# Kernel tuning notes

Measured on AMD Instinct MI355X. Metric: run time of the kernel, lower is better.

The kernel has to match this reference:

```python
import jax, jax.numpy as jnp
import numpy as np

B, CIN, F, H, W = 4, 256, 128, 64, 64
EPS = 1e-5

def _conv1x1(x, Wm, b):
    # x: [B,C,H,W], Wm: [O,C] (1x1 conv kernel), b: [O]
    return jnp.einsum('bchw,oc->bohw', x, Wm) + b[None, :, None, None]

def setup_inputs() -> dict:
    key = jax.random.key(0)
    ks = jax.random.split(key, 11)
    s_in = 1.0 / np.sqrt(CIN)
    s_f = 1.0 / np.sqrt(F)
    return {
        'x':    jax.random.normal(ks[0], (B, CIN, H, W), jnp.float32),
        'Wg':   jax.random.normal(ks[1], (F, CIN), jnp.float32) * s_in,
        'bg':   jax.random.normal(ks[2], (F,), jnp.float32) * s_in,
        'Wt':   jax.random.normal(ks[3], (F, CIN), jnp.float32) * s_in,
        'bt':   jax.random.normal(ks[4], (F,), jnp.float32) * s_in,
        'Wp':   jax.random.normal(ks[5], (F, CIN), jnp.float32) * s_in,
        'bp':   jax.random.normal(ks[6], (F,), jnp.float32) * s_in,
        'Wz':   jax.random.normal(ks[7], (CIN, F), jnp.float32) * s_f,
        'bz':   jax.random.normal(ks[8], (CIN,), jnp.float32) * s_f,
        'ln_w': jax.random.normal(ks[9], (CIN, H, W), jnp.float32) * 0.1,
        'ln_b': jax.random.normal(ks[10], (CIN, H, W), jnp.float32) * 0.1,
    }

def reference(x, Wg, bg, Wt, bt, Wp, bp, Wz, bz, ln_w, ln_b):
    b, _, h, w = x.shape
    n = h * w
    # 1x1 conv projections
    g = _conv1x1(x, Wg, bg).reshape(b, F, n).transpose(0, 2, 1)      # [B,N,F]
    theta = _conv1x1(x, Wt, bt).reshape(b, F, n).transpose(0, 2, 1)  # [B,N,F]
    phi = _conv1x1(x, Wp, bp).reshape(b, F, n)                        # [B,F,N]
    # embedded-Gaussian affinity + softmax attention
    f = jnp.einsum('bnf,bfm->bnm', theta, phi)                        # [B,N,N]
    attn = jax.nn.softmax(f, axis=-1)
    y = jnp.einsum('bnm,bmf->bnf', attn, g)                           # [B,N,F]
    y = y.transpose(0, 2, 1).reshape(b, F, h, w)                      # [B,F,H,W]
    # output projection
    z = _conv1x1(y, Wz, bz)                                           # [B,CIN,H,W]
    # LayerNorm over (C,H,W) per sample, affine params shaped [C,H,W]
    mu = jnp.mean(z, axis=(1, 2, 3), keepdims=True)
    var = jnp.var(z, axis=(1, 2, 3), keepdims=True)
    z = (z - mu) * jax.lax.rsqrt(var + EPS)
    z = z * ln_w[None] + ln_b[None]
    return z + x
```

## Files before the change

### kernel.cpp

```cpp
#include <hip/hip_runtime.h>
#include <stdint.h>

#define CIN 256
#define FDIM 128
#define NSP 4096
#define EPS 1e-5f

typedef __attribute__((ext_vector_type(8))) short short8;
typedef __attribute__((ext_vector_type(4))) float f32x4;
typedef __attribute__((ext_vector_type(16))) float f32x16;

__device__ __forceinline__ short f2bf(float f) {
  union { float f; uint32_t u; } v; v.f = f;
  uint32_t r = v.u + 0x7fffu + ((v.u >> 16) & 1u);
  return (short)(r >> 16);
}
__device__ __forceinline__ float bf2f(short h) {
  union { uint32_t u; float f; } v; v.u = ((uint32_t)(uint16_t)h) << 16;
  return v.f;
}

__global__ void prep_weights(const float* __restrict__ Wg, const float* __restrict__ Wt,
                             const float* __restrict__ Wp, const float* __restrict__ Wz,
                             short* __restrict__ Wbf, short* __restrict__ Wzbf) {
  int idx = blockIdx.x * 256 + threadIdx.x;
  if (idx < 384 * 256) {
    int row = idx >> 8, col = idx & 255;
    float v;
    if (row < 128)       v = Wt[row * 256 + col];
    else if (row < 256)  v = Wp[(row - 128) * 256 + col];
    else                 v = Wg[(row - 256) * 256 + col];
    Wbf[idx] = f2bf(v);
  } else {
    int j = idx - 384 * 256;
    if (j < 256 * 128) Wzbf[j] = f2bf(Wz[j]);
  }
}

__global__ void prep_xT(const float* __restrict__ x, short* __restrict__ xT) {
  __shared__ float tile[32][33];
  int b = blockIdx.z, c0 = blockIdx.y * 32, n0 = blockIdx.x * 32;
  int r = threadIdx.x >> 5, c = threadIdx.x & 31;
  const float* xb = x + (size_t)b * CIN * NSP;
#pragma unroll
  for (int k = 0; k < 4; k++)
    tile[r + 8 * k][c] = xb[(size_t)(c0 + r + 8 * k) * NSP + n0 + c];
  __syncthreads();
  short* xTb = xT + (size_t)b * NSP * CIN;
#pragma unroll
  for (int k = 0; k < 4; k++)
    xTb[(size_t)(n0 + r + 8 * k) * CIN + c0 + c] = f2bf(tile[c][r + 8 * k]);
}

__global__ void __launch_bounds__(256)
proj_kernel(const short* __restrict__ xT, const short* __restrict__ Wbf,
            const float* __restrict__ bt, const float* __restrict__ bp,
            const float* __restrict__ bg,
            short* __restrict__ theta, short* __restrict__ Kb, short* __restrict__ gT) {
  __shared__ short lds[5120];
  int bx = blockIdx.x;
  int b = bx >> 7;
  int n0 = (bx & 127) << 5;
  int p = blockIdx.y;
  int t = threadIdx.x, w = t >> 6, lane = t & 63, l15 = lane & 15, quad = lane >> 4;

  const short* arow = xT + (size_t)(b * NSP + n0 + (w & 1) * 16 + l15) * CIN;
  short8 a[8];
#pragma unroll
  for (int s = 0; s < 8; s++) a[s] = *(const short8*)(arow + s * 32 + quad * 8);

  const short* Wsrc = Wbf + p * 128 * 256;
  f32x4 zero = {0.f, 0.f, 0.f, 0.f};
  f32x4 acc[4];
#pragma unroll
  for (int i = 0; i < 4; i++) acc[i] = zero;

#pragma unroll
  for (int s = 0; s < 8; s++) {
#pragma unroll
    for (int ft = 0; ft < 4; ft++) {
      int ftg = (w >> 1) * 4 + ft;
      short8 bfr = *(const short8*)(Wsrc + (ftg * 16 + l15) * 256 + s * 32 + quad * 8);
      acc[ft] = __builtin_amdgcn_mfma_f32_16x16x32_bf16(a[s], bfr, acc[ft], 0, 0, 0);
    }
  }

  const float* bias = (p == 0) ? bt : (p == 1) ? bp : bg;
  if (p < 2) {
#pragma unroll
    for (int ft = 0; ft < 4; ft++) {
      int ftg = (w >> 1) * 4 + ft;
      float bv = bias[ftg * 16 + l15];
#pragma unroll
      for (int rr = 0; rr < 4; rr++) {
        int n = (w & 1) * 16 + quad * 4 + rr;
        lds[n * 136 + ftg * 16 + l15] = f2bf(acc[ft][rr] + bv);
      }
    }
    __syncthreads();
    short* dst = ((p == 0) ? theta : Kb) + (size_t)(b * NSP + n0) * FDIM;
#pragma unroll
    for (int i = 0; i < 2; i++) {
      int flat = t + 256 * i;
      int row = flat >> 4, ch = flat & 15;
      *(short8*)(dst + (size_t)row * FDIM + ch * 8) = *(const short8*)(lds + row * 136 + ch * 8);
    }
  } else {
#pragma unroll
    for (int ft = 0; ft < 4; ft++) {
      int ftg = (w >> 1) * 4 + ft;
      float bv = bias[ftg * 16 + l15];
#pragma unroll
      for (int rr = 0; rr < 4; rr++) {
        int n = (w & 1) * 16 + quad * 4 + rr;
        lds[(ftg * 16 + l15) * 40 + n] = f2bf(acc[ft][rr] + bv);
      }
    }
    __syncthreads();
    short* dst = gT + (size_t)b * FDIM * NSP + n0;
#pragma unroll
    for (int i = 0; i < 2; i++) {
      int flat = t + 256 * i;
      int f = flat >> 2, c = flat & 3;
      *(short8*)(dst + (size_t)f * NSP + c * 8) = *(const short8*)(lds + f * 40 + c * 8);
    }
  }
}

__global__ void __launch_bounds__(256, 2)
flash_kernel(const short* __restrict__ thetab, const short* __restrict__ Kb,
             const short* __restrict__ gT, short* __restrict__ opart,
             float* __restrict__ lpart) {
  __shared__ __attribute__((aligned(16))) char smem[66048];
  short* KldsA = (short*)smem;
  short* KldsB = (short*)(smem + 8704);
  short* VtA   = (short*)(smem + 17408);
  short* VtB   = (short*)(smem + 27648);
  float* Om    = (float*)smem;
  float* lsm   = (float*)(smem + 65536);

  const int bx = blockIdx.x;
  const int b  = bx >> 7;
  const int r  = bx & 127;
  const int q0 = (r >> 2) << 7;
  const int kc = r & 3;
  const int t = threadIdx.x, w = t >> 6, lane = t & 63;
  const int l31 = lane & 31, h = lane >> 5;
  const int qw = q0 + (w & 1) * 64;

  const short* Qsrc = thetab + (size_t)b * NSP * FDIM;
  const short* Ksrc = Kb + (size_t)b * NSP * FDIM;
  const short* Vsrc = gT + (size_t)b * FDIM * NSP;

  short8 qf0[8], qf1[8];
#pragma unroll
  for (int s = 0; s < 8; s++) {
    qf0[s] = *(const short8*)(Qsrc + (size_t)(qw + l31) * FDIM + s * 16 + h * 8);
    qf1[s] = *(const short8*)(Qsrc + (size_t)(qw + 32 + l31) * FDIM + s * 16 + h * 8);
  }

  f32x16 O0[4], O1[4];
#pragma unroll
  for (int i = 0; i < 4; i++) {
#pragma unroll
    for (int j = 0; j < 16; j++) { O0[i][j] = 0.f; O1[i][j] = 0.f; }
  }
  float lsum0 = 0.f, lsum1 = 0.f;

  const int kA0 = kc << 10;
  for (int j0 = 0; j0 < 512; j0 += 32) {
    __syncthreads();
    int kA = kA0 + j0, kB = kA + 512;
#pragma unroll
    for (int rep = 0; rep < 2; rep++) {
      int flat = t + 256 * rep;
      int row = flat >> 4, c = flat & 15;
      *(short8*)(KldsA + row * 136 + c * 8) =
          *(const short8*)(Ksrc + (size_t)(kA + row) * FDIM + c * 8);
      *(short8*)(KldsB + row * 136 + c * 8) =
          *(const short8*)(Ksrc + (size_t)(kB + row) * FDIM + c * 8);
      int f = flat >> 2, c2 = flat & 3;
      *(short8*)(VtA + f * 40 + c2 * 8) =
          *(const short8*)(Vsrc + (size_t)f * NSP + kA + c2 * 8);
      *(short8*)(VtB + f * 40 + c2 * 8) =
          *(const short8*)(Vsrc + (size_t)f * NSP + kB + c2 * 8);
    }
    __syncthreads();
    const short* Kl = (w & 2) ? KldsB : KldsA;
    const short* Vl = (w & 2) ? VtB : VtA;

    f32x16 S0, S1;
#pragma unroll
    for (int j = 0; j < 16; j++) { S0[j] = 0.f; S1[j] = 0.f; }
#pragma unroll
    for (int s = 0; s < 8; s++) {
      short8 ak = *(const short8*)(Kl + l31 * 136 + s * 16 + h * 8);
      S0 = __builtin_amdgcn_mfma_f32_32x32x16_bf16(ak, qf0[s], S0, 0, 0, 0);
      S1 = __builtin_amdgcn_mfma_f32_32x32x16_bf16(ak, qf1[s], S1, 0, 0, 0);
    }

    short8 Af0[2], Af1[2];
#pragma unroll
    for (int qb = 0; qb < 2; qb++) {
      float p[16];
      float ls = 0.f;
#pragma unroll
      for (int i = 0; i < 16; i++) {
        p[i] = __expf(qb ? S1[i] : S0[i]);
        ls += p[i];
      }
      if (qb) lsum1 += ls; else lsum0 += ls;
#pragma unroll
      for (int tt = 0; tt < 2; tt++) {
        const int rb = tt * 8;
        short8 af;
#pragma unroll
        for (int rr = 0; rr < 4; rr++) {
          float qv = h ? p[rb + rr] : p[rb + 4 + rr];
          float wv = __shfl_xor(qv, 32, 64);
          float e0 = h ? wv : p[rb + rr];
          float e1 = h ? p[rb + 4 + rr] : wv;
          af[rr] = f2bf(e0);
          af[4 + rr] = f2bf(e1);
        }
        if (qb) Af1[tt] = af; else Af0[tt] = af;
      }
    }

#pragma unroll
    for (int ft = 0; ft < 4; ft++) {
#pragma unroll
      for (int tt = 0; tt < 2; tt++) {
        short8 bv = *(const short8*)(Vl + (ft * 32 + l31) * 40 + tt * 16 + h * 8);
        O0[ft] = __builtin_amdgcn_mfma_f32_32x32x16_bf16(Af0[tt], bv, O0[ft], 0, 0, 0);
        O1[ft] = __builtin_amdgcn_mfma_f32_32x32x16_bf16(Af1[tt], bv, O1[ft], 0, 0, 0);
      }
    }
  }

  lsum0 += __shfl_xor(lsum0, 32, 64);
  lsum1 += __shfl_xor(lsum1, 32, 64);

  __syncthreads();
  if (w >= 2) {
    float* dst = Om + (size_t)(w - 2) * 8192;
#pragma unroll
    for (int qb = 0; qb < 2; qb++) {
#pragma unroll
      for (int ft = 0; ft < 4; ft++) {
#pragma unroll
        for (int reg = 0; reg < 16; reg++) {
          int rowq = qb * 32 + (reg & 3) + 8 * (reg >> 2) + 4 * h;
          dst[rowq * 128 + ft * 32 + l31] = qb ? O1[ft][reg] : O0[ft][reg];
        }
      }
    }
    if (h == 0) {
      lsm[(w - 2) * 64 + l31] = lsum0;
      lsm[(w - 2) * 64 + 32 + l31] = lsum1;
    }
  }
  __syncthreads();
  if (w < 2) {
    const float* src = Om + (size_t)w * 8192;
    short* od = opart + ((size_t)(kc * 4 + b) * NSP + qw) * FDIM;
#pragma unroll
    for (int qb = 0; qb < 2; qb++) {
#pragma unroll
      for (int ft = 0; ft < 4; ft++) {
#pragma unroll
        for (int reg = 0; reg < 16; reg++) {
          int rowq = qb * 32 + (reg & 3) + 8 * (reg >> 2) + 4 * h;
          float v = (qb ? O1[ft][reg] : O0[ft][reg]) + src[rowq * 128 + ft * 32 + l31];
          od[(size_t)rowq * FDIM + ft * 32 + l31] = f2bf(v);
        }
      }
    }
    if (h == 0) {
      size_t lb = (size_t)(kc * 4 + b) * NSP + qw;
      lpart[lb + l31] = lsum0 + lsm[w * 64 + l31];
      lpart[lb + 32 + l31] = lsum1 + lsm[w * 64 + 32 + l31];
    }
  }
}

__global__ void __launch_bounds__(256)
zproj_kernel(const short* __restrict__ opart, const float* __restrict__ lpart,
             const short* __restrict__ Wzbf, const float* __restrict__ bz,
             short* __restrict__ zb, float* __restrict__ psums) {
  __shared__ short ldsT[128 * 40];
  __shared__ float wsum[4][2];
  int bx = blockIdx.x;
  int b = bx >> 7;
  int n0 = (bx & 127) << 5;
  int ch0 = blockIdx.y * 128;
  int t = threadIdx.x, w = t >> 6, lane = t & 63, l15 = lane & 15, quad = lane >> 4;

  int row = n0 + (w & 1) * 16 + l15;
  float L = 0.f;
#pragma unroll
  for (int kcc = 0; kcc < 4; kcc++) L += lpart[(size_t)(kcc * 4 + b) * NSP + row];
  float inv = 1.0f / L;

  short8 a[4];
#pragma unroll
  for (int s = 0; s < 4; s++) {
    float accv[8] = {0, 0, 0, 0, 0, 0, 0, 0};
#pragma unroll
    for (int kcc = 0; kcc < 4; kcc++) {
      short8 v = *(const short8*)(opart + ((size_t)(kcc * 4 + b) * NSP + row) * FDIM + s * 32 + quad * 8);
#pragma unroll
      for (int j = 0; j < 8; j++) accv[j] += bf2f(v[j]);
    }
    short8 av;
#pragma unroll
    for (int j = 0; j < 8; j++) av[j] = f2bf(accv[j] * inv);
    a[s] = av;
  }

  f32x4 zero = {0.f, 0.f, 0.f, 0.f};
  f32x4 acc[4];
#pragma unroll
  for (int i = 0; i < 4; i++) acc[i] = zero;
#pragma unroll
  for (int s = 0; s < 4; s++) {
#pragma unroll
    for (int ct = 0; ct < 4; ct++) {
      int co = ch0 + (w >> 1) * 64 + ct * 16 + l15;
      short8 bfr = *(const short8*)(Wzbf + (size_t)co * FDIM + s * 32 + quad * 8);
      acc[ct] = __builtin_amdgcn_mfma_f32_16x16x32_bf16(a[s], bfr, acc[ct], 0, 0, 0);
    }
  }

  float s1 = 0.0f, s2 = 0.0f;
#pragma unroll
  for (int ct = 0; ct < 4; ct++) {
    int cg = (w >> 1) * 64 + ct * 16 + l15;
    float bv = bz[ch0 + cg];
#pragma unroll
    for (int rr = 0; rr < 4; rr++) {
      float v = acc[ct][rr] + bv;
      s1 += v; s2 += v * v;
      ldsT[cg * 40 + (w & 1) * 16 + quad * 4 + rr] = f2bf(v);
    }
  }
#pragma unroll
  for (int off = 32; off >= 1; off >>= 1) {
    s1 += __shfl_xor(s1, off, 64);
    s2 += __shfl_xor(s2, off, 64);
  }
  if (lane == 0) { wsum[w][0] = s1; wsum[w][1] = s2; }
  __syncthreads();
  if (t == 0) {
    int bid = blockIdx.y * 512 + bx;
    psums[bid * 2] = wsum[0][0] + wsum[1][0] + wsum[2][0] + wsum[3][0];
    psums[bid * 2 + 1] = wsum[0][1] + wsum[1][1] + wsum[2][1] + wsum[3][1];
  }
  short* dst = zb + (size_t)b * CIN * NSP + (size_t)ch0 * NSP + n0;
#pragma unroll
  for (int i = 0; i < 2; i++) {
    int flat = t + 256 * i;
    int c = flat >> 2, ch = flat & 3;
    *(short8*)(dst + (size_t)c * NSP + ch * 8) = *(const short8*)(ldsT + c * 40 + ch * 8);
  }
}

__global__ void reduce_sums(const float* __restrict__ psums, float* __restrict__ sums) {
  __shared__ float red[8];
  int t = threadIdx.x;
  if (t < 8) red[t] = 0.f;
  __syncthreads();
  for (int i = t; i < 1024; i += 256) {
    int b = (i & 511) >> 7;
    atomicAdd(&red[b * 2], psums[i * 2]);
    atomicAdd(&red[b * 2 + 1], psums[i * 2 + 1]);
  }
  __syncthreads();
  if (t < 8) sums[t] = red[t];
}

__global__ void __launch_bounds__(256)
finalize_kernel(const short* __restrict__ zbuf, const float* __restrict__ x,
                const float* __restrict__ lnw, const float* __restrict__ lnb,
                const float* __restrict__ sums, float* __restrict__ out) {
  int gid = blockIdx.x * 256 + threadIdx.x;
  size_t e0 = (size_t)gid * 8;
  int b = (int)(e0 >> 20);
  size_t ib = e0 & ((size_t)(1u << 20) - 1);
  float mean = sums[b * 2] * (1.0f / 1048576.0f);
  float var = sums[b * 2 + 1] * (1.0f / 1048576.0f) - mean * mean;
  float rs = rsqrtf(var + EPS);
  short8 zv = *(const short8*)(zbuf + e0);
#pragma unroll
  for (int k = 0; k < 8; k++) {
    float z = bf2f(zv[k]);
    out[e0 + k] = (z - mean) * rs * lnw[ib + k] + lnb[ib + k] + x[e0 + k];
  }
}

extern "C" void kernel_launch(void* const* d_in, const int* in_sizes, int n_in,
                              void* d_out, int out_size, void* d_ws, size_t ws_size,
                              hipStream_t stream) {
  const float* x   = (const float*)d_in[0];
  const float* Wg  = (const float*)d_in[1];
  const float* bg  = (const float*)d_in[2];
  const float* Wt  = (const float*)d_in[3];
  const float* bt  = (const float*)d_in[4];
  const float* Wp  = (const float*)d_in[5];
  const float* bp  = (const float*)d_in[6];
  const float* Wz  = (const float*)d_in[7];
  const float* bz  = (const float*)d_in[8];
  const float* lnw = (const float*)d_in[9];
  const float* lnb = (const float*)d_in[10];
  float* out = (float*)d_out;

  char* ws = (char*)d_ws;
  short* Wbf    = (short*)(ws);
  short* Wzbf   = (short*)(ws + 196608);
  short* xT     = (short*)(ws + 262144);
  short* opart  = (short*)(ws + 262144);
  float* lpart  = (float*)(ws + 17039360);
  short* thetab = (short*)(ws + 17301504);
  short* Kb     = (short*)(ws + 21495808);
  short* gT     = (short*)(ws + 25690112);
  short* zb     = (short*)(ws + 17301504);
  float* sums   = (float*)(ws + 29884416);
  float* psums  = (float*)(ws + 29884448);

  prep_weights<<<512, 256, 0, stream>>>(Wg, Wt, Wp, Wz, Wbf, Wzbf);
  prep_xT<<<dim3(128, 8, 4), 256, 0, stream>>>(x, xT);
  proj_kernel<<<dim3(512, 3), 256, 0, stream>>>(xT, Wbf, bt, bp, bg, thetab, Kb, gT);
  flash_kernel<<<512, 256, 0, stream>>>(thetab, Kb, gT, opart, lpart);
  zproj_kernel<<<dim3(512, 2), 256, 0, stream>>>(opart, lpart, Wzbf, bz, zb, psums);
  reduce_sums<<<1, 256, 0, stream>>>(psums, sums);
  finalize_kernel<<<2048, 256, 0, stream>>>(zb, x, lnw, lnb, sums, out);
}
```

Before: 210.0 us.

## Read K/V directly from global in flash kernel and merge small launches

The flash kernel no longer stages K and V tiles through LDS with two barriers per iteration. Each wave now loads its MFMA operands straight from global memory and walks its own 512-key range. Block indexing is reordered so the four key chunks of a query tile sit next to each other and can share cache. The weight and x-transpose prep kernels are merged into one launch, and the psums reduce kernel is replaced by global atomics after a memset, cutting launch count. The risks are uncoalesced, strided V loads from global, and atomic ordering that makes the summation non-deterministic.

```diff
diff --git a/kernel.cpp b/kernel.cpp
--- a/kernel.cpp
+++ b/kernel.cpp
@@ -20,26 +20,30 @@
   return v.f;
 }
 
-__global__ void prep_weights(const float* __restrict__ Wg, const float* __restrict__ Wt,
-                             const float* __restrict__ Wp, const float* __restrict__ Wz,
-                             short* __restrict__ Wbf, short* __restrict__ Wzbf) {
-  int idx = blockIdx.x * 256 + threadIdx.x;
-  if (idx < 384 * 256) {
-    int row = idx >> 8, col = idx & 255;
-    float v;
-    if (row < 128)       v = Wt[row * 256 + col];
-    else if (row < 256)  v = Wp[(row - 128) * 256 + col];
-    else                 v = Wg[(row - 256) * 256 + col];
-    Wbf[idx] = f2bf(v);
-  } else {
-    int j = idx - 384 * 256;
-    if (j < 256 * 128) Wzbf[j] = f2bf(Wz[j]);
-  }
-}
-
-__global__ void prep_xT(const float* __restrict__ x, short* __restrict__ xT) {
+__global__ void prep_kernel(const float* __restrict__ x,
+                            const float* __restrict__ Wg, const float* __restrict__ Wt,
+                            const float* __restrict__ Wp, const float* __restrict__ Wz,
+                            short* __restrict__ Wbf, short* __restrict__ Wzbf,
+                            short* __restrict__ xT) {
   __shared__ float tile[32][33];
-  int b = blockIdx.z, c0 = blockIdx.y * 32, n0 = blockIdx.x * 32;
+  int bx = blockIdx.x;
+  if (bx < 512) {
+    int idx = bx * 256 + threadIdx.x;
+    if (idx < 384 * 256) {
+      int row = idx >> 8, col = idx & 255;
+      float v;
+      if (row < 128)       v = Wt[row * 256 + col];
+      else if (row < 256)  v = Wp[(row - 128) * 256 + col];
+      else                 v = Wg[(row - 256) * 256 + col];
+      Wbf[idx] = f2bf(v);
+    } else {
+      int j = idx - 384 * 256;
+      if (j < 256 * 128) Wzbf[j] = f2bf(Wz[j]);
+    }
+    return;
+  }
+  int bxx = bx - 512;
+  int n0 = (bxx & 127) * 32, c0 = ((bxx >> 7) & 7) * 32, b = bxx >> 10;
   int r = threadIdx.x >> 5, c = threadIdx.x & 31;
   const float* xb = x + (size_t)b * CIN * NSP;
 #pragma unroll
@@ -131,19 +135,13 @@
 flash_kernel(const short* __restrict__ thetab, const short* __restrict__ Kb,
              const short* __restrict__ gT, short* __restrict__ opart,
              float* __restrict__ lpart) {
-  __shared__ __attribute__((aligned(16))) char smem[66048];
-  short* KldsA = (short*)smem;
-  short* KldsB = (short*)(smem + 8704);
-  short* VtA   = (short*)(smem + 17408);
-  short* VtB   = (short*)(smem + 27648);
-  float* Om    = (float*)smem;
-  float* lsm   = (float*)(smem + 65536);
+  __shared__ float Om[16384];
+  __shared__ float lsm[128];
 
   const int bx = blockIdx.x;
-  const int b  = bx >> 7;
-  const int r  = bx & 127;
-  const int q0 = (r >> 2) << 7;
-  const int kc = r & 3;
+  const int kc = bx & 3;
+  const int b  = (bx >> 2) & 3;
+  const int q0 = (bx >> 4) << 7;
   const int t = threadIdx.x, w = t >> 6, lane = t & 63;
   const int l31 = lane & 31, h = lane >> 5;
   const int qw = q0 + (w & 1) * 64;
@@ -167,34 +165,17 @@
   }
   float lsum0 = 0.f, lsum1 = 0.f;
 
-  const int kA0 = kc << 10;
+  const int kbeg = (kc << 10) + (w >> 1) * 512;
   for (int j0 = 0; j0 < 512; j0 += 32) {
-    __syncthreads();
-    int kA = kA0 + j0, kB = kA + 512;
-#pragma unroll
-    for (int rep = 0; rep < 2; rep++) {
-      int flat = t + 256 * rep;
-      int row = flat >> 4, c = flat & 15;
-      *(short8*)(KldsA + row * 136 + c * 8) =
-          *(const short8*)(Ksrc + (size_t)(kA + row) * FDIM + c * 8);
-      *(short8*)(KldsB + row * 136 + c * 8) =
-          *(const short8*)(Ksrc + (size_t)(kB + row) * FDIM + c * 8);
-      int f = flat >> 2, c2 = flat & 3;
-      *(short8*)(VtA + f * 40 + c2 * 8) =
-          *(const short8*)(Vsrc + (size_t)f * NSP + kA + c2 * 8);
-      *(short8*)(VtB + f * 40 + c2 * 8) =
-          *(const short8*)(Vsrc + (size_t)f * NSP + kB + c2 * 8);
-    }
-    __syncthreads();
-    const short* Kl = (w & 2) ? KldsB : KldsA;
-    const short* Vl = (w & 2) ? VtB : VtA;
+    const int kk = kbeg + j0;
 
     f32x16 S0, S1;
 #pragma unroll
     for (int j = 0; j < 16; j++) { S0[j] = 0.f; S1[j] = 0.f; }
+    const short* Kp = Ksrc + (size_t)(kk + l31) * FDIM + h * 8;
 #pragma unroll
     for (int s = 0; s < 8; s++) {
-      short8 ak = *(const short8*)(Kl + l31 * 136 + s * 16 + h * 8);
+      short8 ak = *(const short8*)(Kp + s * 16);
       S0 = __builtin_amdgcn_mfma_f32_32x32x16_bf16(ak, qf0[s], S0, 0, 0, 0);
       S1 = __builtin_amdgcn_mfma_f32_32x32x16_bf16(ak, qf1[s], S1, 0, 0, 0);
     }
@@ -229,9 +210,10 @@
 
 #pragma unroll
     for (int ft = 0; ft < 4; ft++) {
+      const short* Vp = Vsrc + (size_t)(ft * 32 + l31) * NSP + kk + h * 8;
 #pragma unroll
       for (int tt = 0; tt < 2; tt++) {
-        short8 bv = *(const short8*)(Vl + (ft * 32 + l31) * 40 + tt * 16 + h * 8);
+        short8 bv = *(const short8*)(Vp + tt * 16);
         O0[ft] = __builtin_amdgcn_mfma_f32_32x32x16_bf16(Af0[tt], bv, O0[ft], 0, 0, 0);
         O1[ft] = __builtin_amdgcn_mfma_f32_32x32x16_bf16(Af1[tt], bv, O1[ft], 0, 0, 0);
       }
@@ -287,7 +269,7 @@
 __global__ void __launch_bounds__(256)
 zproj_kernel(const short* __restrict__ opart, const float* __restrict__ lpart,
              const short* __restrict__ Wzbf, const float* __restrict__ bz,
-             short* __restrict__ zb, float* __restrict__ psums) {
+             short* __restrict__ zb, float* __restrict__ sums) {
   __shared__ short ldsT[128 * 40];
   __shared__ float wsum[4][2];
   int bx = blockIdx.x;
@@ -352,9 +334,8 @@
   if (lane == 0) { wsum[w][0] = s1; wsum[w][1] = s2; }
   __syncthreads();
   if (t == 0) {
-    int bid = blockIdx.y * 512 + bx;
-    psums[bid * 2] = wsum[0][0] + wsum[1][0] + wsum[2][0] + wsum[3][0];
-    psums[bid * 2 + 1] = wsum[0][1] + wsum[1][1] + wsum[2][1] + wsum[3][1];
+    atomicAdd(&sums[b * 2], wsum[0][0] + wsum[1][0] + wsum[2][0] + wsum[3][0]);
+    atomicAdd(&sums[b * 2 + 1], wsum[0][1] + wsum[1][1] + wsum[2][1] + wsum[3][1]);
   }
   short* dst = zb + (size_t)b * CIN * NSP + (size_t)ch0 * NSP + n0;
 #pragma unroll
@@ -363,20 +344,6 @@
     int c = flat >> 2, ch = flat & 3;
     *(short8*)(dst + (size_t)c * NSP + ch * 8) = *(const short8*)(ldsT + c * 40 + ch * 8);
   }
-}
-
-__global__ void reduce_sums(const float* __restrict__ psums, float* __restrict__ sums) {
-  __shared__ float red[8];
-  int t = threadIdx.x;
-  if (t < 8) red[t] = 0.f;
-  __syncthreads();
-  for (int i = t; i < 1024; i += 256) {
-    int b = (i & 511) >> 7;
-    atomicAdd(&red[b * 2], psums[i * 2]);
-    atomicAdd(&red[b * 2 + 1], psums[i * 2 + 1]);
-  }
-  __syncthreads();
-  if (t < 8) sums[t] = red[t];
 }
 
 __global__ void __launch_bounds__(256)
@@ -425,13 +392,11 @@
   short* gT     = (short*)(ws + 25690112);
   short* zb     = (short*)(ws + 17301504);
   float* sums   = (float*)(ws + 29884416);
-  float* psums  = (float*)(ws + 29884448);
-
-  prep_weights<<<512, 256, 0, stream>>>(Wg, Wt, Wp, Wz, Wbf, Wzbf);
-  prep_xT<<<dim3(128, 8, 4), 256, 0, stream>>>(x, xT);
+
+  hipMemsetAsync(sums, 0, 8 * sizeof(float), stream);
+  prep_kernel<<<4608, 256, 0, stream>>>(x, Wg, Wt, Wp, Wz, Wbf, Wzbf, xT);
   proj_kernel<<<dim3(512, 3), 256, 0, stream>>>(xT, Wbf, bt, bp, bg, thetab, Kb, gT);
   flash_kernel<<<512, 256, 0, stream>>>(thetab, Kb, gT, opart, lpart);
-  zproj_kernel<<<dim3(512, 2), 256, 0, stream>>>(opart, lpart, Wzbf, bz, zb, psums);
-  reduce_sums<<<1, 256, 0, stream>>>(psums, sums);
+  zproj_kernel<<<dim3(512, 2), 256, 0, stream>>>(opart, lpart, Wzbf, bz, zb, sums);
   finalize_kernel<<<2048, 256, 0, stream>>>(zb, x, lnw, lnb, sums, out);
 }
```

Result: slower. 258.0 us (+22.9%).
